# Kernel tuning notes

Measured on AMD Instinct MI355X. Metric: run time of the kernel, lower is better.

Reference implementation:

```python
import jax, jax.numpy as jnp
import numpy as np

IN_DIM = 1024
OUT_DIM = 1024
L = 4
HIDDEN = 64
EMB_DIM = 2 + 2 * 2 * L  # 18
BATCH = 8192
W0 = 30.0


def make_embedded_coords():
    gy, gx = jnp.meshgrid(jnp.linspace(-1.0, 1.0, OUT_DIM), jnp.linspace(-1.0, 1.0, IN_DIM), indexing='ij')
    coords = jnp.stack([gy, gx], axis=-1).reshape(-1, 2)  # [rows*cols, 2]
    embeds = [coords]
    for i in range(L):
        freq = 2.0 ** i
        embeds.append(jnp.sin(freq * jnp.pi * coords))
        embeds.append(jnp.cos(freq * jnp.pi * coords))
    return jnp.concatenate(embeds, axis=-1)  # [rows*cols, 18]


def setup_inputs() -> dict:
    key = jax.random.key(0)
    ks = jax.random.split(key, 8)
    # init scales matching torch code
    u = lambda k, shape, b: jax.random.uniform(k, shape, jnp.float32, -b, b)
    W1 = u(ks[0], (HIDDEN, EMB_DIM), 1.0 / EMB_DIM)
    b1 = u(ks[1], (HIDDEN,), 1.0 / np.sqrt(EMB_DIM))
    s2 = np.sqrt(6.0 / HIDDEN) / W0
    W2 = u(ks[2], (HIDDEN, HIDDEN), s2)
    b2 = u(ks[3], (HIDDEN,), 1.0 / np.sqrt(HIDDEN))
    W3 = u(ks[4], (1, HIDDEN), s2)
    b3 = u(ks[5], (1,), 1.0 / np.sqrt(HIDDEN))
    x = jax.random.normal(ks[6], (BATCH, IN_DIM), jnp.float32)
    bias = jnp.zeros((OUT_DIM,), jnp.float32)
    return {
        'x': x,
        'embedded_coords': make_embedded_coords(),
        'W1': W1, 'b1': b1, 'W2': W2, 'b2': b2, 'W3': W3, 'b3': b3,
        'bias': bias,
    }


def reference(x, embedded_coords, W1, b1, W2, b2, W3, b3, bias):
    rows = bias.shape[0]
    cols = x.shape[-1]
    # tiny fully-fused hypernet MLP over rows*cols coordinate points
    h = jnp.sin(W0 * (embedded_coords @ W1.T + b1))  # [rows*cols, 64]
    h = jnp.sin(W0 * (h @ W2.T + b2))                # [rows*cols, 64]
    W = (h @ W3.T + b3).reshape(rows, cols)          # generated weight
    return x @ W.T + bias                            # [batch, out_dim]
```

## Files before the change

kernel.cpp:

```cpp
#include <hip/hip_runtime.h>
#include <hip/hip_bf16.h>


typedef __attribute__((ext_vector_type(8))) short bf16x8;
typedef __attribute__((ext_vector_type(4))) float f32x4;

__device__ __forceinline__ unsigned short f2bf(float f) {
    union { float f; unsigned u; } v; v.f = f;
    unsigned r = v.u + 0x7fffu + ((v.u >> 16) & 1u);
    return (unsigned short)(r >> 16);
}

__device__ __forceinline__ void async_ld16(const void* g, void* l) {
    __builtin_amdgcn_global_load_lds(
        (__attribute__((address_space(1))) void*)g,
        (__attribute__((address_space(3))) void*)l, 16, 0, 0);
}

__global__ __launch_bounds__(256) void cast_x_kernel(
        const float4* __restrict__ x, unsigned short* __restrict__ xb) {
    long i = (long)blockIdx.x * 256 + threadIdx.x;
    float4 v = x[i];
    ushort4 o;
    o.x = f2bf(v.x); o.y = f2bf(v.y); o.z = f2bf(v.z); o.w = f2bf(v.w);
    *(ushort4*)(xb + i * 4) = o;
}

__global__ __launch_bounds__(256) void siren_tables_kernel(
        const float* __restrict__ ec,
        const float* __restrict__ W1, const float* __restrict__ b1,
        float* __restrict__ Zrow, float* __restrict__ Zcol) {
    int t = blockIdx.x * 256 + threadIdx.x;
    float e[18];
    if (t < 1024) {
        const float* pe = ec + (long)t * 1024 * 18;
        #pragma unroll
        for (int i = 0; i < 18; ++i) e[i] = pe[i];
        for (int j = 0; j < 64; ++j) {
            float z = b1[j];
            #pragma unroll
            for (int i = 0; i < 18; ++i) z += W1[j * 18 + i] * e[i];
            Zrow[t * 64 + j] = z;
        }
    } else {
        int c = t - 1024;
        const float* pe = ec + (long)c * 18;
        #pragma unroll
        for (int i = 0; i < 18; ++i) e[i] = pe[i] - ec[i];
        for (int j = 0; j < 64; ++j) {
            float z = 0.f;
            #pragma unroll
            for (int i = 0; i < 18; ++i) z += W1[j * 18 + i] * e[i];
            Zcol[c * 64 + j] = z;
        }
    }
}

__global__ __launch_bounds__(256, 4) void siren_w_kernel(
        const float* __restrict__ Zrow, const float* __restrict__ Zcol,
        const float* __restrict__ W2, const float* __restrict__ b2,
        const float* __restrict__ W3, const float* __restrict__ b3,
        unsigned short* __restrict__ Wout) {
    int lane = threadIdx.x & 63;
    int wv   = threadIdx.x >> 6;
    int ln   = lane & 15;
    int kq   = lane >> 4;

    bf16x8 bfrag[2][4];
    #pragma unroll
    for (int kc = 0; kc < 2; ++kc)
        #pragma unroll
        for (int nt = 0; nt < 4; ++nt) {
            const float* src = W2 + (nt * 16 + ln) * 64 + kc * 32 + kq * 8;
            union { bf16x8 v; unsigned short u[8]; } tmp;
            #pragma unroll
            for (int j = 0; j < 8; ++j) tmp.u[j] = f2bf(src[j]);
            bfrag[kc][nt] = tmp.v;
        }
    float b2v[4], w3v[4];
    #pragma unroll
    for (int nt = 0; nt < 4; ++nt) {
        b2v[nt] = b2[nt * 16 + ln];
        w3v[nt] = W3[nt * 16 + ln];
    }
    float b3s = b3[0];

    long wave_id = (long)blockIdx.x * 4 + wv;
    for (int it = 0; it < 16; ++it) {
        long tile = wave_id * 16 + it;
        long p0 = tile * 16;
        int r = (int)(p0 >> 10);
        int c = (int)(p0 & 1023) + ln;

        const float* zc = Zcol + (long)c * 64 + kq * 8;
        const float* zr = Zrow + (long)r * 64 + kq * 8;
        union { bf16x8 v; unsigned short u[8]; } a0, a1;
        #pragma unroll
        for (int j = 0; j < 8; ++j) {
            a0.u[j] = f2bf(__sinf(30.f * (zr[j] + zc[j])));
            a1.u[j] = f2bf(__sinf(30.f * (zr[32 + j] + zc[32 + j])));
        }

        f32x4 acc[4] = {};
        #pragma unroll
        for (int nt = 0; nt < 4; ++nt) {
            acc[nt] = __builtin_amdgcn_mfma_f32_16x16x32_bf16(a0.v, bfrag[0][nt], acc[nt], 0, 0, 0);
            acc[nt] = __builtin_amdgcn_mfma_f32_16x16x32_bf16(a1.v, bfrag[1][nt], acc[nt], 0, 0, 0);
        }

        float part[4];
        #pragma unroll
        for (int rg = 0; rg < 4; ++rg) {
            float s = 0.f;
            #pragma unroll
            for (int nt = 0; nt < 4; ++nt)
                s += w3v[nt] * __sinf(30.f * (acc[nt][rg] + b2v[nt]));
            part[rg] = s;
        }
        #pragma unroll
        for (int m = 1; m < 16; m <<= 1)
            #pragma unroll
            for (int rg = 0; rg < 4; ++rg)
                part[rg] += __shfl_xor(part[rg], m, 64);

        if (ln == 0) {
            ushort4 o;
            o.x = f2bf(part[0] + b3s);
            o.y = f2bf(part[1] + b3s);
            o.z = f2bf(part[2] + b3s);
            o.w = f2bf(part[3] + b3s);
            *(ushort4*)(Wout + p0 + kq * 4) = o;
        }
    }
}

__global__ __launch_bounds__(256) void gemm_kernel(
        const unsigned short* __restrict__ A,
        const unsigned short* __restrict__ B,
        const float* __restrict__ bias,
        float* __restrict__ C) {
    const int K = 1024;
    __shared__ __align__(16) unsigned short As[128 * 32];
    __shared__ __align__(16) unsigned short Bs[128 * 32];

    int tid  = threadIdx.x;
    int lane = tid & 63;
    int wv   = tid >> 6;
    int wm   = wv & 1, wn = wv >> 1;
    long Abase = (long)blockIdx.x * 128 * K;
    long Bbase = (long)blockIdx.y * 128 * K;

    int sr = tid >> 2;
    int sc = tid & 3;
    int rsel = lane & 15;
    int csel = lane >> 4;

    f32x4 acc[4][4] = {};

    for (int kt = 0; kt < K; kt += 32) {
        #pragma unroll
        for (int q = 0; q < 2; ++q) {
            int row = q * 64 + sr;
            int cc  = sc ^ ((row >> 1) & 3);
            const unsigned short* ga = A + Abase + (long)row * K + kt + cc * 8;
            const unsigned short* gb = B + Bbase + (long)row * K + kt + cc * 8;
            unsigned short* la = &As[(q * 256 + wv * 64) * 8];
            unsigned short* lb = &Bs[(q * 256 + wv * 64) * 8];
            async_ld16(ga, la);
            async_ld16(gb, lb);
        }
        __syncthreads();

        bf16x8 af[4], bf[4];
        #pragma unroll
        for (int mi = 0; mi < 4; ++mi) {
            int row = wm * 64 + mi * 16 + rsel;
            int ch  = csel ^ ((row >> 1) & 3);
            af[mi] = *(const bf16x8*)&As[row * 32 + ch * 8];
        }
        #pragma unroll
        for (int ni = 0; ni < 4; ++ni) {
            int row = wn * 64 + ni * 16 + rsel;
            int ch  = csel ^ ((row >> 1) & 3);
            bf[ni] = *(const bf16x8*)&Bs[row * 32 + ch * 8];
        }
        #pragma unroll
        for (int mi = 0; mi < 4; ++mi)
            #pragma unroll
            for (int ni = 0; ni < 4; ++ni)
                acc[mi][ni] = __builtin_amdgcn_mfma_f32_16x16x32_bf16(
                    af[mi], bf[ni], acc[mi][ni], 0, 0, 0);
        __syncthreads();
    }

    int row0 = blockIdx.x * 128 + wm * 64;
    int col0 = blockIdx.y * 128 + wn * 64;
    #pragma unroll
    for (int ni = 0; ni < 4; ++ni) {
        int col = col0 + ni * 16 + rsel;
        float bv = bias[col];
        #pragma unroll
        for (int mi = 0; mi < 4; ++mi) {
            int rbase = row0 + mi * 16 + csel * 4;
            #pragma unroll
            for (int r = 0; r < 4; ++r)
                C[(long)(rbase + r) * 1024 + col] = acc[mi][ni][r] + bv;
        }
    }
}

extern "C" void kernel_launch(void* const* d_in, const int* in_sizes, int n_in,
                              void* d_out, int out_size, void* d_ws, size_t ws_size,
                              hipStream_t stream) {
    const float* x    = (const float*)d_in[0];
    const float* ec   = (const float*)d_in[1];
    const float* W1   = (const float*)d_in[2];
    const float* b1   = (const float*)d_in[3];
    const float* W2   = (const float*)d_in[4];
    const float* b2   = (const float*)d_in[5];
    const float* W3   = (const float*)d_in[6];
    const float* b3   = (const float*)d_in[7];
    const float* bias = (const float*)d_in[8];
    float* out = (float*)d_out;

    unsigned short* xb = (unsigned short*)d_ws;
    unsigned short* Wb = xb + (size_t)8192 * 1024;
    float* Zrow = (float*)(Wb + (size_t)1024 * 1024);
    float* Zcol = Zrow + 1024 * 64;

    cast_x_kernel<<<8192, 256, 0, stream>>>((const float4*)x, xb);
    siren_tables_kernel<<<8, 256, 0, stream>>>(ec, W1, b1, Zrow, Zcol);
    siren_w_kernel<<<1024, 256, 0, stream>>>(Zrow, Zcol, W2, b2, W3, b3, Wb);
    dim3 g(64, 8);
    gemm_kernel<<<g, 256, 0, stream>>>(xb, Wb, bias, out);
}
```

Before: 225.2 us.

## Parallelize SIREN table kernel per output and fold W0 scaling into tables

The first-layer table kernel now uses one thread per (point, hidden unit) across 512 blocks instead of 2048 threads each doing 64 serial outputs, removing a badly underparallelised launch. The W0=30 factor is folded into Zrow, Zcol, W2 and b2, which drops multiplies from the inner loop. The weight kernel assigns each wave one row with its Zrow values held in registers, running 8 iterations over 2048 blocks. Float-to-bf16 conversion of the activations and W2 now uses packed truncation instead of round-to-nearest-even, which adds a small precision risk.

Result: faster. 215.6 us (-4.3%).

```diff
diff --git a/kernel.cpp b/kernel.cpp
--- a/kernel.cpp
+++ b/kernel.cpp
@@ -9,6 +9,11 @@
     union { float f; unsigned u; } v; v.f = f;
     unsigned r = v.u + 0x7fffu + ((v.u >> 16) & 1u);
     return (unsigned short)(r >> 16);
+}
+
+__device__ __forceinline__ unsigned pktrunc(float a, float b) {
+    union { float f; unsigned u; } x, y; x.f = a; y.f = b;
+    return (x.u >> 16) | (y.u & 0xffff0000u);
 }
 
 __device__ __forceinline__ void async_ld16(const void* g, void* l) {
@@ -30,29 +35,23 @@
         const float* __restrict__ ec,
         const float* __restrict__ W1, const float* __restrict__ b1,
         float* __restrict__ Zrow, float* __restrict__ Zcol) {
-    int t = blockIdx.x * 256 + threadIdx.x;
-    float e[18];
+    int idx = blockIdx.x * 256 + threadIdx.x;
+    int j = idx & 63;
+    int t = idx >> 6;
+    const float* wr = W1 + j * 18;
     if (t < 1024) {
         const float* pe = ec + (long)t * 1024 * 18;
-        #pragma unroll
-        for (int i = 0; i < 18; ++i) e[i] = pe[i];
-        for (int j = 0; j < 64; ++j) {
-            float z = b1[j];
-            #pragma unroll
-            for (int i = 0; i < 18; ++i) z += W1[j * 18 + i] * e[i];
-            Zrow[t * 64 + j] = z;
-        }
+        float z = b1[j];
+        #pragma unroll
+        for (int i = 0; i < 18; ++i) z += wr[i] * pe[i];
+        Zrow[t * 64 + j] = 30.f * z;
     } else {
         int c = t - 1024;
         const float* pe = ec + (long)c * 18;
-        #pragma unroll
-        for (int i = 0; i < 18; ++i) e[i] = pe[i] - ec[i];
-        for (int j = 0; j < 64; ++j) {
-            float z = 0.f;
-            #pragma unroll
-            for (int i = 0; i < 18; ++i) z += W1[j * 18 + i] * e[i];
-            Zcol[c * 64 + j] = z;
-        }
+        float z = 0.f;
+        #pragma unroll
+        for (int i = 0; i < 18; ++i) z += wr[i] * (pe[i] - ec[i]);
+        Zcol[c * 64 + j] = 30.f * z;
     }
 }
 
@@ -72,33 +71,44 @@
         #pragma unroll
         for (int nt = 0; nt < 4; ++nt) {
             const float* src = W2 + (nt * 16 + ln) * 64 + kc * 32 + kq * 8;
-            union { bf16x8 v; unsigned short u[8]; } tmp;
-            #pragma unroll
-            for (int j = 0; j < 8; ++j) tmp.u[j] = f2bf(src[j]);
+            union { bf16x8 v; unsigned u[4]; } tmp;
+            #pragma unroll
+            for (int q = 0; q < 4; ++q)
+                tmp.u[q] = pktrunc(30.f * src[2*q], 30.f * src[2*q + 1]);
             bfrag[kc][nt] = tmp.v;
         }
     float b2v[4], w3v[4];
     #pragma unroll
     for (int nt = 0; nt < 4; ++nt) {
-        b2v[nt] = b2[nt * 16 + ln];
+        b2v[nt] = 30.f * b2[nt * 16 + ln];
         w3v[nt] = W3[nt * 16 + ln];
     }
     float b3s = b3[0];
 
-    long wave_id = (long)blockIdx.x * 4 + wv;
-    for (int it = 0; it < 16; ++it) {
-        long tile = wave_id * 16 + it;
-        long p0 = tile * 16;
-        int r = (int)(p0 >> 10);
-        int c = (int)(p0 & 1023) + ln;
-
+    int wid = blockIdx.x * 4 + wv;
+    int r   = wid >> 3;
+    int c0  = (wid & 7) * 128;
+
+    const float* zrp = Zrow + (long)r * 64 + kq * 8;
+    float zr0[8], zr1[8];
+    #pragma unroll
+    for (int j = 0; j < 8; ++j) { zr0[j] = zrp[j]; zr1[j] = zrp[32 + j]; }
+
+    for (int it = 0; it < 8; ++it) {
+        int c = c0 + it * 16 + ln;
         const float* zc = Zcol + (long)c * 64 + kq * 8;
-        const float* zr = Zrow + (long)r * 64 + kq * 8;
-        union { bf16x8 v; unsigned short u[8]; } a0, a1;
+
+        float s0[8], s1[8];
         #pragma unroll
         for (int j = 0; j < 8; ++j) {
-            a0.u[j] = f2bf(__sinf(30.f * (zr[j] + zc[j])));
-            a1.u[j] = f2bf(__sinf(30.f * (zr[32 + j] + zc[32 + j])));
+            s0[j] = __sinf(zr0[j] + zc[j]);
+            s1[j] = __sinf(zr1[j] + zc[32 + j]);
+        }
+        union { bf16x8 v; unsigned u[4]; } a0, a1;
+        #pragma unroll
+        for (int q = 0; q < 4; ++q) {
+            a0.u[q] = pktrunc(s0[2*q], s0[2*q + 1]);
+            a1.u[q] = pktrunc(s1[2*q], s1[2*q + 1]);
         }
 
         f32x4 acc[4] = {};
@@ -114,7 +124,7 @@
             float s = 0.f;
             #pragma unroll
             for (int nt = 0; nt < 4; ++nt)
-                s += w3v[nt] * __sinf(30.f * (acc[nt][rg] + b2v[nt]));
+                s += w3v[nt] * __sinf(acc[nt][rg] + b2v[nt]);
             part[rg] = s;
         }
         #pragma unroll
@@ -124,6 +134,7 @@
                 part[rg] += __shfl_xor(part[rg], m, 64);
 
         if (ln == 0) {
+            long p0 = (long)r * 1024 + c0 + it * 16;
             ushort4 o;
             o.x = f2bf(part[0] + b3s);
             o.y = f2bf(part[1] + b3s);
@@ -229,8 +240,8 @@
     float* Zcol = Zrow + 1024 * 64;
 
     cast_x_kernel<<<8192, 256, 0, stream>>>((const float4*)x, xb);
-    siren_tables_kernel<<<8, 256, 0, stream>>>(ec, W1, b1, Zrow, Zcol);
-    siren_w_kernel<<<1024, 256, 0, stream>>>(Zrow, Zcol, W2, b2, W3, b3, Wb);
+    siren_tables_kernel<<<512, 256, 0, stream>>>(ec, W1, b1, Zrow, Zcol);
+    siren_w_kernel<<<2048, 256, 0, stream>>>(Zrow, Zcol, W2, b2, W3, b3, Wb);
     dim3 g(64, 8);
     gemm_kernel<<<g, 256, 0, stream>>>(xb, Wb, bias, out);
 }
```
